# Performance work log

Hardware: AMD Instinct MI355X
Metric: run time of the kernel (lower is better)

Reference implementation:

```python
import jax, jax.numpy as jnp
import numpy as np

N = 50000          # num nodes
E = 800000         # num edges (avg degree 16)
C_IN = 64          # input channels
TOWERS = 4
F_IN = C_IN // TOWERS       # 16 (divide_input=True)
OUT = 128
F_OUT = OUT // TOWERS       # 32
NUM_AGG = 4                 # mean, std, max, min
NUM_SC = 3                  # identity, amplification, attenuation
AVG_LOG_DEG = float(np.log(17.0))  # deg histogram: all nodes degree 16 -> log(16+1)


def setup_inputs() -> dict:
    key = jax.random.key(0)
    ks = jax.random.split(key, 10)
    nodes = jax.random.normal(ks[0], (N, C_IN), dtype=jnp.float32)
    senders = jax.random.randint(ks[1], (E,), 0, N)
    receivers = jax.random.randint(ks[2], (E,), 0, N)
    # per-tower pre-MLP: Linear(2*F_IN -> F_IN), pre_layers=1 (no activation)
    pre_w = jax.random.normal(ks[3], (TOWERS, 2 * F_IN, F_IN), dtype=jnp.float32) / np.sqrt(2 * F_IN)
    pre_b = jnp.zeros((TOWERS, F_IN), dtype=jnp.float32)
    # per-tower post-MLP: Linear(F_IN + F_IN*12 -> F_OUT), post_layers=1
    post_in = F_IN + F_IN * NUM_AGG * NUM_SC  # 208
    post_w = jax.random.normal(ks[4], (TOWERS, post_in, F_OUT), dtype=jnp.float32) / np.sqrt(post_in)
    post_b = jnp.zeros((TOWERS, F_OUT), dtype=jnp.float32)
    # final linear: TOWERS*F_OUT -> OUT
    lin_w = jax.random.normal(ks[5], (TOWERS * F_OUT, OUT), dtype=jnp.float32) / np.sqrt(TOWERS * F_OUT)
    lin_b = jnp.zeros((OUT,), dtype=jnp.float32)
    return {"nodes": nodes, "senders": senders, "receivers": receivers,
            "pre_w": pre_w, "pre_b": pre_b, "post_w": post_w, "post_b": post_b,
            "lin_w": lin_w, "lin_b": lin_b}


def reference(nodes, senders, receivers, pre_w, pre_b, post_w, post_b, lin_w, lin_b):
    # divide_input=True: split channels across towers -> [N, T, F_IN]
    x = nodes.reshape(N, TOWERS, F_IN)
    x_i = x[senders]                                  # [E, T, F_IN]
    x_j = x[receivers]                                # [E, T, F_IN]
    h = jnp.concatenate([x_i, x_j], axis=-1)          # [E, T, 2*F_IN]
    # per-tower pre-MLP (single linear), vectorized over towers
    msg = jnp.einsum('etf,tfo->eto', h, pre_w) + pre_b  # [E, T, F_IN]

    # degree-scaled multi-aggregator segment reduce over receivers
    count = jax.ops.segment_sum(jnp.ones((E,), dtype=msg.dtype), receivers, num_segments=N)  # [N]
    d = jnp.clip(count, 1.0, None)
    inv_d = (1.0 / d)[:, None, None]
    mean = jax.ops.segment_sum(msg, receivers, num_segments=N) * inv_d           # [N,T,F]
    mean_sq = jax.ops.segment_sum(msg * msg, receivers, num_segments=N) * inv_d
    std = jnp.sqrt(jax.nn.relu(mean_sq - mean * mean) + 1e-5)
    has_nb = (count > 0)[:, None, None]
    mx = jax.ops.segment_max(msg, receivers, num_segments=N)
    mx = jnp.where(has_nb, mx, 0.0)
    mn = -jax.ops.segment_max(-msg, receivers, num_segments=N)
    mn = jnp.where(has_nb, mn, 0.0)
    agg = jnp.concatenate([mean, std, mx, mn], axis=-1)  # [N, T, 4*F_IN]

    # scalers: identity, amplification, attenuation (degree clamped to >= 1)
    log_d = jnp.log(d + 1.0)[:, None, None]
    amp = log_d / AVG_LOG_DEG
    att = AVG_LOG_DEG / log_d
    scaled = jnp.concatenate([agg, agg * amp, agg * att], axis=-1)  # [N, T, 12*F_IN]

    out = jnp.concatenate([x, scaled], axis=-1)                     # [N, T, 13*F_IN]
    outs = jnp.einsum('ntf,tfo->nto', out, post_w) + post_b         # [N, T, F_OUT]
    flat = outs.reshape(N, TOWERS * F_OUT)                          # [N, 128]
    return flat @ lin_w + lin_b                                     # [N, OUT]
```

## Files before the change

### kernel.cpp

```cpp
#include <hip/hip_runtime.h>

#define AVG_LOG_DEG 2.8332133440562162f
#define CAP 64

typedef __attribute__((ext_vector_type(8))) short short8;
typedef __attribute__((ext_vector_type(4))) float f32x4;

static __device__ __forceinline__ float bl(unsigned u) { return __uint_as_float(u << 16); }
static __device__ __forceinline__ float bh(unsigned u) { return __uint_as_float(u & 0xffff0000u); }
static __device__ __forceinline__ unsigned short f2b(float f) {
    unsigned u = __float_as_uint(f);
    return (unsigned short)((u + 0x7fffu + ((u >> 16) & 1u)) >> 16);
}
static __device__ __forceinline__ unsigned pk(unsigned short lo, unsigned short hi) {
    return (unsigned)lo | ((unsigned)hi << 16);
}


__global__ __launch_bounds__(256) void k_setup(
    const float* __restrict__ nodes, const float* __restrict__ pre_w,
    const float* __restrict__ pre_b,
    const float* __restrict__ post_w, const float* __restrict__ lin_w,
    unsigned short* __restrict__ Yh, float* __restrict__ H,
    unsigned short* __restrict__ postT,
    unsigned short* __restrict__ linT, int* __restrict__ cursor,
    int n, int A, int nbN)
{
    int b = blockIdx.x;
    if (b < A) {
        int lane = threadIdx.x & 63;
        int node = b * 4 + (threadIdx.x >> 6);
        if (node >= n) return;
        int t = lane >> 4, f = lane & 15;
        float w0[16], w1[16];
        #pragma unroll
        for (int k = 0; k < 16; ++k) {
            w0[k] = pre_w[(t * 32 + k) * 16 + f];
            w1[k] = pre_w[(t * 32 + 16 + k) * 16 + f];
        }
        const float4* xp = reinterpret_cast<const float4*>(nodes + (size_t)node * 64 + t * 16);
        float4 x0 = xp[0], x1 = xp[1], x2 = xp[2], x3 = xp[3];
        float xs[16] = {x0.x, x0.y, x0.z, x0.w, x1.x, x1.y, x1.z, x1.w,
                        x2.x, x2.y, x2.z, x2.w, x3.x, x3.y, x3.z, x3.w};
        float y = 0.f;
        float h = pre_b[t * 16 + f];
        #pragma unroll
        for (int k = 0; k < 16; ++k) {
            y = fmaf(xs[k], w0[k], y);
            h = fmaf(xs[k], w1[k], h);
        }
        Yh[(size_t)node * 64 + lane] = f2b(y);
        H[(size_t)node * 64 + lane] = h;
    } else if (b < A + 176) {
        int i = (b - A) * 256 + threadIdx.x;
        if (i < 28672) {
            int t = i / (32 * 224);
            int r = i % (32 * 224);
            int nn = r / 224;
            int k = r % 224;
            float wv;
            if (k < 192)      wv = post_w[((size_t)t * 208 + 16 + k) * 32 + nn];
            else if (k < 208) wv = post_w[((size_t)t * 208 + (k - 192)) * 32 + nn];
            else              wv = 0.f;
            postT[i] = f2b(wv);
        }
        int j = i - 28672;
        if (j >= 0 && j < 16384) {
            int nn = j >> 7, k = j & 127;
            linT[j] = f2b(lin_w[k * 128 + nn]);
        }
    } else {
        int i = (b - A - 176) * 256 + threadIdx.x;
        if (i < n) cursor[i] = 0;
    }
}


__global__ __launch_bounds__(256) void k_scatter2(
    const int* __restrict__ send, const int* __restrict__ recv,
    int* __restrict__ cursor, int* __restrict__ slots,
    int e, int nps)
{
    int slice = blockIdx.x & 7;
    int chunk = blockIdx.x >> 3;
    int base = chunk * 4096 + threadIdx.x * 4;
    int lo = slice * nps;
    int4 rv[4];
    #pragma unroll
    for (int it = 0; it < 4; ++it) {
        int i = base + it * 1024;
        if (i + 3 < e) {
            rv[it] = *reinterpret_cast<const int4*>(recv + i);
        } else {
            rv[it].x = rv[it].y = rv[it].z = rv[it].w = -1;
            #pragma unroll
            for (int q = 0; q < 4; ++q)
                if (i + q < e) ((int*)&rv[it])[q] = recv[i + q];
        }
    }
    #pragma unroll
    for (int it = 0; it < 4; ++it) {
        int i = base + it * 1024;
        int rr[4] = {rv[it].x, rv[it].y, rv[it].z, rv[it].w};
        #pragma unroll
        for (int q = 0; q < 4; ++q) {
            int r = rr[q];
            if ((unsigned)(r - lo) < (unsigned)nps) {
                int p = atomicAdd(&cursor[r], 1);
                if (p < CAP) slots[(size_t)r * CAP + p] = send[i + q];
            }
        }
    }
}


__global__ __launch_bounds__(256) void k_agg(
    const int* __restrict__ cursor,
    const int* __restrict__ slots,
    const unsigned short* __restrict__ Yh,
    const float* __restrict__ H,
    unsigned short* __restrict__ aggh, int n)
{
    int lane = threadIdx.x & 63;
    int node = blockIdx.x * 4 + (threadIdx.x >> 6);
    if (node >= n) return;
    int t = lane >> 4, f = lane & 15;

    int idxv = slots[(size_t)node * CAP + lane];
    float hjw = H[(size_t)node * 64 + lane];
    int d = min(cursor[node], CAP);
    const unsigned short* Yl = Yh + lane;

    float s = 0.f, s2 = 0.f, mx = -INFINITY, mn = INFINITY;
    int e = 0;
    for (; e + 16 <= d; e += 16) {
        unsigned v[16];
        #pragma unroll
        for (int q = 0; q < 16; ++q) {
            int si = __builtin_amdgcn_readlane(idxv, e + q);
            v[q] = Yl[(size_t)si * 64];
        }
        #pragma unroll
        for (int q = 0; q < 16; ++q) {
            float m = __uint_as_float(v[q] << 16) + hjw;
            s += m;
            s2 = fmaf(m, m, s2);
            mx = fmaxf(mx, m);
            mn = fminf(mn, m);
        }
    }
    int rem = d - e;
    if (rem > 0) {
        unsigned v[16];
        #pragma unroll
        for (int q = 0; q < 16; ++q) {
            int si = __builtin_amdgcn_readlane(idxv, min(e + q, d - 1));
            v[q] = Yl[(size_t)si * 64];
        }
        #pragma unroll
        for (int q = 0; q < 16; ++q) {
            if (q < rem) {
                float m = __uint_as_float(v[q] << 16) + hjw;
                s += m;
                s2 = fmaf(m, m, s2);
                mx = fmaxf(mx, m);
                mn = fminf(mn, m);
            }
        }
    }

    float dc = fmaxf((float)d, 1.f);
    float inv = 1.f / dc;
    float mean = s * inv;
    float var = fmaf(-mean, mean, s2 * inv);
    float sd = sqrtf(fmaxf(var, 0.f) + 1e-5f);
    if (d == 0) { mx = 0.f; mn = 0.f; }

    unsigned short* ag = aggh + (size_t)node * 256 + t * 64 + f;
    ag[0]  = f2b(mean);
    ag[16] = f2b(sd);
    ag[32] = f2b(mx);
    ag[48] = f2b(mn);
}


__global__ __launch_bounds__(256, 3) void k_post(
    const float* __restrict__ nodes,
    const unsigned short* __restrict__ aggh,
    const int* __restrict__ deg,
    const unsigned short* __restrict__ postT,
    const unsigned short* __restrict__ linT,
    const float* __restrict__ post_b,
    const float* __restrict__ lin_b,
    float* __restrict__ out, int n)
{
    __shared__ unsigned short sV[32 * 256];
    __shared__ unsigned short sFlat[32 * 128];
    __shared__ float sAmp[32], sAtt[32];

    int tid = threadIdx.x;
    int n0 = blockIdx.x * 32;

    if (tid < 32) {
        int g = min(n0 + tid, n - 1);
        float dc = fmaxf((float)min(deg[g], CAP), 1.f);
        float ld = logf(dc + 1.f);
        sAmp[tid] = ld * (1.f / AVG_LOG_DEG);
        sAtt[tid] = AVG_LOG_DEG / ld;
    }

    int w = tid >> 6, lane = tid & 63;
    int quad = lane >> 4, mr = lane & 15;
    int mstrip = w & 1, nhalf = w >> 1;
    int nn = tid >> 3, j8 = tid & 7;
    int sw = nn & 7;
    int gn = min(n0 + nn, n - 1);
    int rsw = mr & 7;

    uint4 pa4[4];
    #pragma unroll
    for (int t = 0; t < 4; ++t)
        pa4[t] = *reinterpret_cast<const uint4*>(aggh + (size_t)gn * 256 + t * 64 + j8 * 8);

    uint4 xw4[4];
    #pragma unroll
    for (int t = 0; t < 4; ++t) { xw4[t].x = 0; xw4[t].y = 0; xw4[t].z = 0; xw4[t].w = 0; }
    if (j8 < 2) {
        #pragma unroll
        for (int t = 0; t < 4; ++t) {
            const float4* xp = reinterpret_cast<const float4*>(nodes + (size_t)gn * 64 + t * 16 + j8 * 8);
            float4 xa = xp[0], xb = xp[1];
            xw4[t].x = pk(f2b(xa.x), f2b(xa.y)); xw4[t].y = pk(f2b(xa.z), f2b(xa.w));
            xw4[t].z = pk(f2b(xb.x), f2b(xb.y)); xw4[t].w = pk(f2b(xb.z), f2b(xb.w));
        }
    }

    const unsigned short* bbase = postT + (size_t)(nhalf * 16 + mr) * 224 + quad * 8;
    short8 bA[7], bB[7];
    #pragma unroll
    for (int kk = 0; kk < 7; ++kk) bA[kk] = *reinterpret_cast<const short8*>(bbase + kk * 32);
    #pragma unroll
    for (int kk = 0; kk < 7; ++kk) bB[kk] = *reinterpret_cast<const short8*>(bbase + 32 * 224 + kk * 32);

    __syncthreads();
    float ampv = sAmp[nn], attv = sAtt[nn];

    #pragma unroll
    for (int t = 0; t < 4; ++t) {
        {
            unsigned short* row = &sV[nn * 256];
            uint4 a = pa4[t];
            *reinterpret_cast<uint4*>(row + (j8 ^ sw) * 8) = a;
            unsigned uu[4] = {a.x, a.y, a.z, a.w};
            unsigned short pa[8], pb[8];
            #pragma unroll
            for (int q = 0; q < 4; ++q) {
                float lo = bl(uu[q]), hi = bh(uu[q]);
                pa[2*q]   = f2b(lo * ampv); pa[2*q+1] = f2b(hi * ampv);
                pb[2*q]   = f2b(lo * attv); pb[2*q+1] = f2b(hi * attv);
            }
            uint4 wa, wb;
            wa.x = pk(pa[0], pa[1]); wa.y = pk(pa[2], pa[3]);
            wa.z = pk(pa[4], pa[5]); wa.w = pk(pa[6], pa[7]);
            wb.x = pk(pb[0], pb[1]); wb.y = pk(pb[2], pb[3]);
            wb.z = pk(pb[4], pb[5]); wb.w = pk(pb[6], pb[7]);
            *reinterpret_cast<uint4*>(row + (8  + (j8 ^ sw)) * 8) = wa;
            *reinterpret_cast<uint4*>(row + (16 + (j8 ^ sw)) * 8) = wb;
            *reinterpret_cast<uint4*>(row + (24 + (j8 ^ sw)) * 8) = xw4[t];
        }
        __syncthreads();

        f32x4 acc = {0.f, 0.f, 0.f, 0.f};
        const unsigned short* av0 = &sV[(mstrip * 16 + mr) * 256];
        #pragma unroll
        for (int kk = 0; kk < 7; ++kk) {
            int c = kk * 4 + quad;
            int pc = (c & ~7) | ((c & 7) ^ rsw);
            short8 avv = *reinterpret_cast<const short8*>(av0 + pc * 8);
            if (t & 1) acc = __builtin_amdgcn_mfma_f32_16x16x32_bf16(avv, bB[kk], acc, 0, 0, 0);
            else       acc = __builtin_amdgcn_mfma_f32_16x16x32_bf16(avv, bA[kk], acc, 0, 0, 0);
        }

        if (t == 0) {
            #pragma unroll
            for (int kk = 0; kk < 7; ++kk)
                bA[kk] = *reinterpret_cast<const short8*>(bbase + 2 * 32 * 224 + kk * 32);
        } else if (t == 1) {
            #pragma unroll
            for (int kk = 0; kk < 7; ++kk)
                bB[kk] = *reinterpret_cast<const short8*>(bbase + 3 * 32 * 224 + kk * 32);
        }

        int col = t * 32 + nhalf * 16 + mr;
        float pbv = post_b[col];
        int cc = col >> 3, co = col & 7;
        #pragma unroll
        for (int i = 0; i < 4; ++i) {
            int rowf = mstrip * 16 + quad * 4 + i;
            int pc = (cc & ~7) | ((cc & 7) ^ (rowf & 7));
            sFlat[rowf * 128 + pc * 8 + co] = f2b(acc[i] + pbv);
        }
        __syncthreads();
    }

    f32x4 facc[4];
    #pragma unroll
    for (int nt = 0; nt < 4; ++nt) { facc[nt].x = 0.f; facc[nt].y = 0.f; facc[nt].z = 0.f; facc[nt].w = 0.f; }

    const unsigned short* af0 = &sFlat[(mstrip * 16 + mr) * 128];
    #pragma unroll
    for (int kk = 0; kk < 4; ++kk) {
        int c = kk * 4 + quad;
        int pc = (c & ~7) | ((c & 7) ^ rsw);
        short8 avv = *reinterpret_cast<const short8*>(af0 + pc * 8);
        #pragma unroll
        for (int nt = 0; nt < 4; ++nt) {
            short8 bv = *reinterpret_cast<const short8*>(
                linT + (size_t)(nhalf * 64 + nt * 16 + mr) * 128 + kk * 32 + quad * 8);
            facc[nt] = __builtin_amdgcn_mfma_f32_16x16x32_bf16(avv, bv, facc[nt], 0, 0, 0);
        }
    }

    #pragma unroll
    for (int nt = 0; nt < 4; ++nt) {
        int col = nhalf * 64 + nt * 16 + mr;
        float lb = lin_b[col];
        #pragma unroll
        for (int i = 0; i < 4; ++i) {
            int node = n0 + mstrip * 16 + quad * 4 + i;
            if (node < n) out[(size_t)node * 128 + col] = facc[nt][i] + lb;
        }
    }
}

extern "C" void kernel_launch(void* const* d_in, const int* in_sizes, int n_in,
                              void* d_out, int out_size, void* d_ws, size_t ws_size,
                              hipStream_t stream)
{
    const float* nodes  = (const float*)d_in[0];
    const int*   send   = (const int*)d_in[1];
    const int*   recv   = (const int*)d_in[2];
    const float* pre_w  = (const float*)d_in[3];
    const float* pre_b  = (const float*)d_in[4];
    const float* post_w = (const float*)d_in[5];
    const float* post_b = (const float*)d_in[6];
    const float* lin_w  = (const float*)d_in[7];
    const float* lin_b  = (const float*)d_in[8];
    float* out = (float*)d_out;

    int N = in_sizes[0] / 64;
    int E = in_sizes[1];
    int Npad = (N + 255) & ~255;

    int* cursor = (int*)d_ws;
    int* slots  = cursor + Npad;
    unsigned short* Yh = (unsigned short*)(slots + (size_t)Npad * CAP);
    float* H = (float*)(Yh + (size_t)Npad * 64);
    unsigned short* aggh  = (unsigned short*)(H + (size_t)Npad * 64);
    unsigned short* postT = aggh + (size_t)Npad * 256;
    unsigned short* linT  = postT + 28672;

    int nbN = (N + 255) / 256;
    int A = (N + 3) / 4;
    int nps = (N + 7) / 8;
    int nbS = 8 * ((E + 4095) / 4096);

    k_setup   <<<A + 176 + nbN, 256, 0, stream>>>(nodes, pre_w, pre_b, post_w, lin_w,
                                                  Yh, H, postT, linT, cursor, N, A, nbN);
    k_scatter2<<<nbS, 256, 0, stream>>>(send, recv, cursor, slots, E, nps);
    k_agg     <<<(N + 3) / 4, 256, 0, stream>>>(cursor, slots, Yh, H, aggh, N);
    k_post    <<<(N + 31) / 32, 256, 0, stream>>>(nodes, aggh, cursor, postT, linT,
                                                  post_b, lin_b, out, N);
}
```

Before: 206.5 us.

## Pad per-node atomic counters to 64-byte stride and shrink scatter blocks

Each node's degree counter now sits at a 16-int stride, so concurrent atomics from the scatter kernel land on separate 64-byte regions instead of sharing cache lines. The scatter kernel also processes 4 edges per thread instead of 16, issuing all its atomics before any slot writes, and launches four times as many blocks. The cost is a 16x larger counter array to zero in setup and strided, uncoalesced counter reads in the aggregation and post kernels.

```diff
diff --git a/kernel.cpp b/kernel.cpp
--- a/kernel.cpp
+++ b/kernel.cpp
@@ -2,6 +2,7 @@
 
 #define AVG_LOG_DEG 2.8332133440562162f
 #define CAP 64
+#define CSTRIDE 16
 
 typedef __attribute__((ext_vector_type(8))) short short8;
 typedef __attribute__((ext_vector_type(4))) float f32x4;
@@ -24,7 +25,7 @@
     unsigned short* __restrict__ Yh, float* __restrict__ H,
     unsigned short* __restrict__ postT,
     unsigned short* __restrict__ linT, int* __restrict__ cursor,
-    int n, int A, int nbN)
+    int n, int A, int n16)
 {
     int b = blockIdx.x;
     if (b < A) {
@@ -70,8 +71,11 @@
             linT[j] = f2b(lin_w[k * 128 + nn]);
         }
     } else {
-        int i = (b - A - 176) * 256 + threadIdx.x;
-        if (i < n) cursor[i] = 0;
+        int i = (b - A - 176) * 1024 + threadIdx.x * 4;
+        if (i < n16) {
+            int4 z; z.x = z.y = z.z = z.w = 0;
+            *reinterpret_cast<int4*>(cursor + i) = z;
+        }
     }
 }
 
@@ -83,33 +87,30 @@
 {
     int slice = blockIdx.x & 7;
     int chunk = blockIdx.x >> 3;
-    int base = chunk * 4096 + threadIdx.x * 4;
+    int i0 = chunk * 1024 + (threadIdx.x << 2);
     int lo = slice * nps;
-    int4 rv[4];
-    #pragma unroll
-    for (int it = 0; it < 4; ++it) {
-        int i = base + it * 1024;
-        if (i + 3 < e) {
-            rv[it] = *reinterpret_cast<const int4*>(recv + i);
-        } else {
-            rv[it].x = rv[it].y = rv[it].z = rv[it].w = -1;
-            #pragma unroll
-            for (int q = 0; q < 4; ++q)
-                if (i + q < e) ((int*)&rv[it])[q] = recv[i + q];
-        }
-    }
-    #pragma unroll
-    for (int it = 0; it < 4; ++it) {
-        int i = base + it * 1024;
-        int rr[4] = {rv[it].x, rv[it].y, rv[it].z, rv[it].w};
-        #pragma unroll
-        for (int q = 0; q < 4; ++q) {
-            int r = rr[q];
-            if ((unsigned)(r - lo) < (unsigned)nps) {
-                int p = atomicAdd(&cursor[r], 1);
-                if (p < CAP) slots[(size_t)r * CAP + p] = send[i + q];
-            }
-        }
+    int4 rv;
+    if (i0 + 3 < e) {
+        rv = *reinterpret_cast<const int4*>(recv + i0);
+    } else {
+        rv.x = rv.y = rv.z = rv.w = -1;
+        #pragma unroll
+        for (int q = 0; q < 4; ++q)
+            if (i0 + q < e) ((int*)&rv)[q] = recv[i0 + q];
+    }
+    int rr[4] = {rv.x, rv.y, rv.z, rv.w};
+    int pv[4];
+    bool m[4];
+    #pragma unroll
+    for (int q = 0; q < 4; ++q) {
+        m[q] = (unsigned)(rr[q] - lo) < (unsigned)nps;
+        pv[q] = 0;
+        if (m[q]) pv[q] = atomicAdd(&cursor[(size_t)rr[q] * CSTRIDE], 1);
+    }
+    #pragma unroll
+    for (int q = 0; q < 4; ++q) {
+        if (m[q] && pv[q] < CAP)
+            slots[(size_t)rr[q] * CAP + pv[q]] = send[i0 + q];
     }
 }
 
@@ -128,7 +129,7 @@
 
     int idxv = slots[(size_t)node * CAP + lane];
     float hjw = H[(size_t)node * 64 + lane];
-    int d = min(cursor[node], CAP);
+    int d = min(cursor[(size_t)node * CSTRIDE], CAP);
     const unsigned short* Yl = Yh + lane;
 
     float s = 0.f, s2 = 0.f, mx = -INFINITY, mn = INFINITY;
@@ -203,7 +204,7 @@
 
     if (tid < 32) {
         int g = min(n0 + tid, n - 1);
-        float dc = fmaxf((float)min(deg[g], CAP), 1.f);
+        float dc = fmaxf((float)min(deg[(size_t)g * CSTRIDE], CAP), 1.f);
         float ld = logf(dc + 1.f);
         sAmp[tid] = ld * (1.f / AVG_LOG_DEG);
         sAtt[tid] = AVG_LOG_DEG / ld;
@@ -353,20 +354,21 @@
     int Npad = (N + 255) & ~255;
 
     int* cursor = (int*)d_ws;
-    int* slots  = cursor + Npad;
+    int* slots  = cursor + (size_t)Npad * CSTRIDE;
     unsigned short* Yh = (unsigned short*)(slots + (size_t)Npad * CAP);
     float* H = (float*)(Yh + (size_t)Npad * 64);
     unsigned short* aggh  = (unsigned short*)(H + (size_t)Npad * 64);
     unsigned short* postT = aggh + (size_t)Npad * 256;
     unsigned short* linT  = postT + 28672;
 
-    int nbN = (N + 255) / 256;
+    int n16 = Npad * CSTRIDE;
+    int nbZ = (n16 + 1023) / 1024;
     int A = (N + 3) / 4;
     int nps = (N + 7) / 8;
-    int nbS = 8 * ((E + 4095) / 4096);
-
-    k_setup   <<<A + 176 + nbN, 256, 0, stream>>>(nodes, pre_w, pre_b, post_w, lin_w,
-                                                  Yh, H, postT, linT, cursor, N, A, nbN);
+    int nbS = 8 * ((E + 1023) / 1024);
+
+    k_setup   <<<A + 176 + nbZ, 256, 0, stream>>>(nodes, pre_w, pre_b, post_w, lin_w,
+                                                  Yh, H, postT, linT, cursor, N, A, n16);
     k_scatter2<<<nbS, 256, 0, stream>>>(send, recv, cursor, slots, E, nps);
     k_agg     <<<(N + 3) / 4, 256, 0, stream>>>(cursor, slots, Yh, H, aggh, N);
     k_post    <<<(N + 31) / 32, 256, 0, stream>>>(nodes, aggh, cursor, postT, linT,
```

Result: faster. 202.5 us (-2.0%).
